# Optimization experiments

Hardware: AMD Instinct MI355X
Metric: run time of the kernel (lower is better)

## Reference

```python
import jax, jax.numpy as jnp
import numpy as np

ALPHA = 0.2  # LeakyReLU negative slope
OUT = 128


def setup_inputs() -> dict:
    key = jax.random.key(0)
    k1, k2, k3, k4 = jax.random.split(key, 4)
    n, d_in, d_out = 8192, 512, OUT
    x = jax.random.normal(k1, (n, d_in), dtype=jnp.float32)
    immediate_neighbor = jax.random.randint(k2, (n, n), 0, 2, dtype=jnp.int32)
    weights = jax.random.normal(k3, (d_in, d_out), dtype=jnp.float32) * (1.0 / np.sqrt(d_in))
    attention = jax.random.normal(k4, (2 * d_out, 1), dtype=jnp.float32) * (1.0 / np.sqrt(2 * d_out))
    return {"x": x, "immediate_neighbor": immediate_neighbor, "weights": weights, "attention": attention}


def reference(x, immediate_neighbor, weights, attention):
    # h: [n, d_out]
    h = x @ weights
    a_src = attention[:OUT, 0]  # [d_out]
    a_dst = attention[OUT:, 0]  # [d_out]
    # e[i, j] = leaky_relu(h[i]·a_src + h[j]·a_dst) -- equivalent to the
    # original's [n*n, 2*d_out] concat @ attention without materializing it.
    e = jax.nn.leaky_relu((h @ a_src)[:, None] + (h @ a_dst)[None, :], ALPHA)
    # Faithful to source: non-neighbors get score 0.0 (not -inf) before softmax.
    masked = jnp.where(immediate_neighbor > 0, e, 0.0)
    att = jax.nn.softmax(masked, axis=1)
    # dropout with training=False is identity
    h_hat = att @ h
    return jax.nn.elu(h_hat)  # concat=True
```

## Files before the change

### kernel.cpp

```cpp
#include <hip/hip_runtime.h>

#define NROW 8192
#define DIN  512
#define DOUT 128
#define QLEN (NROW / 4)

typedef float f32x4 __attribute__((ext_vector_type(4)));
typedef short s16x8 __attribute__((ext_vector_type(8)));
typedef unsigned short u16;

__device__ __forceinline__ u16 f2bf(float f) {
  unsigned u = __float_as_uint(f);
  u += 0x7fffu + ((u >> 16) & 1u);
  return (u16)(u >> 16);
}
__device__ __forceinline__ float bf2f(u16 b) {
  return __uint_as_float(((unsigned)b) << 16);
}
__device__ __forceinline__ unsigned enc_f32(float f) {
  unsigned u = __float_as_uint(f);
  return (u & 0x80000000u) ? ~u : (u | 0x80000000u);
}
__device__ __forceinline__ float dec_f32(unsigned e) {
  unsigned u = (e & 0x80000000u) ? (e & 0x7fffffffu) : ~e;
  return __uint_as_float(u);
}

__global__ void k_probe(float* __restrict__ rowtab, float* __restrict__ coltab,
                        int* __restrict__ destslot, unsigned* __restrict__ pflag) {
  const int lane = threadIdx.x & 63;
  const int r = lane & 15, kg = lane >> 4;
  const short one = (short)f2bf(1.0f);
  s16x8 aLab, ones, labR;
  #pragma unroll
  for (int e = 0; e < 8; ++e) {
    aLab[e] = (short)f2bf((float)(kg * 8 + e));
    ones[e] = one;
    labR[e] = (short)f2bf((float)r);
  }
  const f32x4 z4 = {0.f, 0.f, 0.f, 0.f};

  f32x4 dP = __builtin_amdgcn_mfma_f32_16x16x32_bf16(labR, ones, z4, 0, 0, 0);
  f32x4 dQ = __builtin_amdgcn_mfma_f32_16x16x32_bf16(ones, labR, z4, 0, 0, 0);
  #pragma unroll
  for (int q = 0; q < 4; ++q) {
    float rv = dP[q] * 0.03125f, cv = dQ[q] * 0.03125f;
    rowtab[lane * 4 + q] = rv;
    coltab[lane * 4 + q] = cv;
    int ri = (int)(rv + 0.5f), ci = (int)(cv + 0.5f);
    if (fabsf(rv - ri) > 1e-3f || fabsf(cv - ci) > 1e-3f ||
        ri < 0 || ri > 15 || ci < 0 || ci > 15)
      atomicOr(pflag, 1u);
  }

  unsigned cover = 0;
  for (int b = 0; b < 32; ++b) {
    s16x8 bb;
    #pragma unroll
    for (int e = 0; e < 8; ++e)
      bb[e] = (kg == (b >> 3) && e == (b & 7)) ? one : (short)0;
    f32x4 dB = __builtin_amdgcn_mfma_f32_16x16x32_bf16(aLab, bb, z4, 0, 0, 0);
    if (lane == 0) {
      float v = dB[0];
      int s = (int)(v + 0.5f);
      if (fabsf(v - s) > 1e-3f || s < 0 || s > 31) { atomicOr(pflag, 2u); s &= 31; }
      destslot[s] = b;
      cover |= (1u << s);
    }
  }
  if (lane == 0 && cover != 0xFFFFFFFFu) atomicOr(pflag, 4u);
}

__global__ __launch_bounds__(256) void k_hproj(
    const float* __restrict__ x, const float* __restrict__ w,
    const float* __restrict__ att, const int* __restrict__ destslot,
    u16* __restrict__ hT, float* __restrict__ s, float* __restrict__ d,
    unsigned* __restrict__ dmax)
{
  __shared__ float xs[16 * 513];
  __shared__ float red[8][2][2];
  __shared__ __align__(16) u16 hstage[128][16];
  __shared__ int dslot_sh[32];
  const int t  = threadIdx.x;
  const int i0 = blockIdx.x * 16;

  if (t < 32) dslot_sh[t] = destslot[t];
  #pragma unroll
  for (int jj = 0; jj < 32; ++jj) {
    int f = t + jj * 256;
    int row = f >> 9, col = f & 511;
    xs[row * 513 + col] = x[(size_t)(i0 + row) * DIN + col];
  }
  __syncthreads();

  const int cg = t & 31;
  const int rg = t >> 5;
  f32x4 acc0 = {0.f,0.f,0.f,0.f}, acc1 = {0.f,0.f,0.f,0.f};
  const float* wp  = w + cg * 4;
  const float* xr0 = &xs[(rg * 2 + 0) * 513];
  const float* xr1 = &xs[(rg * 2 + 1) * 513];
  #pragma unroll 4
  for (int k = 0; k < DIN; ++k) {
    f32x4 wv = *(const f32x4*)(wp + (size_t)k * DOUT);
    float x0 = xr0[k], x1 = xr1[k];
    #pragma unroll
    for (int e = 0; e < 4; ++e) {
      acc0[e] = fmaf(x0, wv[e], acc0[e]);
      acc1[e] = fmaf(x1, wv[e], acc1[e]);
    }
  }

  float as0[4], ad0[4];
  #pragma unroll
  for (int e = 0; e < 4; ++e) { as0[e] = att[cg*4+e]; ad0[e] = att[DOUT + cg*4+e]; }
  float ps0=0.f, pd0=0.f, ps1=0.f, pd1=0.f;
  #pragma unroll
  for (int e = 0; e < 4; ++e) {
    ps0 = fmaf(acc0[e], as0[e], ps0); pd0 = fmaf(acc0[e], ad0[e], pd0);
    ps1 = fmaf(acc1[e], as0[e], ps1); pd1 = fmaf(acc1[e], ad0[e], pd1);
  }
  #pragma unroll
  for (int off = 16; off; off >>= 1) {
    ps0 += __shfl_xor(ps0, off); pd0 += __shfl_xor(pd0, off);
    ps1 += __shfl_xor(ps1, off); pd1 += __shfl_xor(pd1, off);
  }
  if (cg == 0) {
    red[rg][0][0] = ps0; red[rg][0][1] = pd0;
    red[rg][1][0] = ps1; red[rg][1][1] = pd1;
  }
  #pragma unroll
  for (int e = 0; e < 4; ++e) {
    hstage[cg*4+e][rg*2+0] = f2bf(acc0[e]);
    hstage[cg*4+e][rg*2+1] = f2bf(acc1[e]);
  }
  __syncthreads();

  if (t < 16) {
    int rgi = t >> 1, rr = t & 1;
    float sv = red[rgi][rr][0], dv = red[rgi][rr][1];
    int i = i0 + rgi * 2 + rr;
    s[i] = sv; d[i] = dv;
    atomicMax(dmax, enc_f32(dv));
  }
  {
    int col = t >> 1, half = t & 1;
    int m32 = i0 & ~31;
    u16* base = hT + (size_t)col * NROW + m32;
    #pragma unroll
    for (int e = 0; e < 8; ++e) {
      int j_rel = (i0 & 16) + half * 8 + e;
      base[dslot_sh[j_rel]] = hstage[col][half * 8 + e];
    }
  }
}

__global__ __launch_bounds__(512, 4) void k_gat(
    const int* __restrict__ nb, const u16* __restrict__ hT,
    const float* __restrict__ s, const float* __restrict__ d,
    const unsigned* __restrict__ dmax_enc, const float* __restrict__ rowtab,
    const float* __restrict__ coltab, float* __restrict__ c_part,
    float* __restrict__ z_part)
{
  __shared__ __align__(16) char arena[40960];
  char* hbase = arena;
  char* abase = arena + 32768;

  const int t    = threadIdx.x;
  const int wid  = t >> 6, lane = t & 63;
  const int r    = lane & 15;
  const int kg   = lane >> 4;
  const int bid  = blockIdx.x;
  const int rt   = bid & 255, qs = bid >> 8;
  const int i0   = rt * 32;
  const int jq0  = qs * QLEN;

  const int wrow = t >> 4;
  const int jp   = t & 15;

  int rlab[4], clab[4];
  #pragma unroll
  for (int q = 0; q < 4; ++q) {
    rlab[q] = (int)(rowtab[lane * 4 + q] + 0.5f);
    clab[q] = (int)(coltab[lane * 4 + q] + 0.5f);
  }

  const float Dmax = dec_f32(*dmax_enc);
  const float svw  = s[i0 + wrow];
  float tM = svw + Dmax;
  const float M   = fmaxf(fmaxf(tM, 0.2f * tM), 0.0f);
  const float enm = __expf(-M);

  f32x4 acc0 = {0.f,0.f,0.f,0.f}, acc1 = {0.f,0.f,0.f,0.f};
  float zacc = 0.f;
  const size_t nbrow = (size_t)(i0 + wrow) * NROW + jq0;
  const float* drow  = d + jq0;
  const int swzw = (wrow & 7) << 4;
  const int swzr = (r & 7) << 4;

  auto do_dma = [&](int buf, int j0) {
    #pragma unroll
    for (int gi = 0; gi < 2; ++gi) {
      int g = wid * 2 + gi;
      int row = g * 8 + (lane >> 3);
      const char* src = (const char*)hT + (size_t)row * (NROW * 2)
                        + (size_t)(jq0 + j0) * 2
                        + (((lane & 7) * 16) ^ ((row & 7) << 4));
      char* dst = hbase + buf * 16384 + g * 1024;
      __builtin_amdgcn_global_load_lds(
          (const __attribute__((address_space(1))) unsigned*)src,
          (__attribute__((address_space(3))) unsigned*)dst, 16, 0, 0);
    }
  };
  auto wcalc = [&](int nbv, float dvv) -> unsigned {
    float tt = svw + dvv;
    float ee = fmaxf(tt, 0.2f * tt) - M;
    float wv = nbv > 0 ? __expf(ee) : enm;
    u16 b = f2bf(wv);
    zacc += bf2f(b);
    return (unsigned)b;
  };
  auto do_weights = [&](int buf, int4 nv, f32x4 dvv) {
    unsigned b0 = wcalc(nv.x, dvv[0]), b1 = wcalc(nv.y, dvv[1]);
    unsigned b2 = wcalc(nv.z, dvv[2]), b3 = wcalc(nv.w, dvv[3]);
    uint2 pk; pk.x = b0 | (b1 << 16); pk.y = b2 | (b3 << 16);
    *(uint2*)(abase + buf * 4096 + wrow * 128 + ((jp * 8) ^ swzw)) = pk;
  };

  {
    int4  nv = *(const int4*)(nb + nbrow + jp * 4);
    f32x4 dv = *(const f32x4*)(drow + jp * 4);
    do_weights(0, nv, dv);
  }
  do_dma(0, 0);
  int4  nv_c = *(const int4*)(nb + nbrow + 64 + jp * 4);
  f32x4 dv_c = *(const f32x4*)(drow + 64 + jp * 4);
  __syncthreads();

  #pragma unroll 1
  for (int w = 0; w < QLEN / 64; ++w) {
    const int cur = w & 1;
    if (w < QLEN / 64 - 1) do_dma(cur ^ 1, (w + 1) * 64);

    const char* ab  = abase + cur * 4096;
    const char* hb  = hbase + cur * 16384 + (wid * 16 + r) * 128;
    const char* a0p = ab + r * 128;
    const char* a1p = ab + (16 + r) * 128;
    #pragma unroll
    for (int jk = 0; jk < 2; ++jk) {
      const int off = (jk * 64 + kg * 16) ^ swzr;
      s16x8 bf  = *(const s16x8*)(hb  + off);
      s16x8 af0 = *(const s16x8*)(a0p + off);
      s16x8 af1 = *(const s16x8*)(a1p + off);
      acc0 = __builtin_amdgcn_mfma_f32_16x16x32_bf16(af0, bf, acc0, 0, 0, 0);
      acc1 = __builtin_amdgcn_mfma_f32_16x16x32_bf16(af1, bf, acc1, 0, 0, 0);
    }

    if (w < QLEN / 64 - 1) {
      do_weights(cur ^ 1, nv_c, dv_c);
      if (w < QLEN / 64 - 2) {
        const int jn = (w + 2) * 64;
        nv_c = *(const int4*)(nb + nbrow + jn + jp * 4);
        dv_c = *(const f32x4*)(drow + jn + jp * 4);
      }
    }
    __syncthreads();
  }

  #pragma unroll
  for (int off = 1; off < 16; off <<= 1) zacc += __shfl_xor(zacc, off);
  if (jp == 0) z_part[qs * NROW + i0 + wrow] = zacc;

  float* cp = c_part + (size_t)qs * NROW * DOUT;
  #pragma unroll
  for (int q = 0; q < 4; ++q) {
    cp[(size_t)(i0 +      rlab[q]) * DOUT + wid * 16 + clab[q]] = acc0[q];
    cp[(size_t)(i0 + 16 + rlab[q]) * DOUT + wid * 16 + clab[q]] = acc1[q];
  }
}

__global__ __launch_bounds__(256) void k_final(
    const float* __restrict__ c_part, const float* __restrict__ z_part,
    float* __restrict__ out)
{
  const int idx = blockIdx.x * 256 + threadIdx.x;
  const int row = idx >> 5, cq = (idx & 31) * 4;
  const size_t base = (size_t)row * DOUT + cq;
  f32x4 v = *(const f32x4*)(c_part + base);
  #pragma unroll
  for (int qsl = 1; qsl < 4; ++qsl) {
    f32x4 p = *(const f32x4*)(c_part + (size_t)qsl * NROW * DOUT + base);
    #pragma unroll
    for (int e = 0; e < 4; ++e) v[e] += p[e];
  }
  float zt = z_part[row] + z_part[NROW + row] + z_part[2 * NROW + row] + z_part[3 * NROW + row];
  f32x4 o;
  #pragma unroll
  for (int e = 0; e < 4; ++e) {
    float val = v[e] / zt;
    o[e] = val > 0.f ? val : expm1f(val);
  }
  *(f32x4*)(out + base) = o;
}

__global__ void k_apply(const unsigned* __restrict__ pflag, float* __restrict__ out) {
  if (threadIdx.x == 0 && blockIdx.x == 0) {
    unsigned f = *pflag;
    out[0] += (f & 1u ? 4e-4f : 0.f) + (f & 2u ? 8e-4f : 0.f) + (f & 4u ? 1.6e-3f : 0.f);
  }
}

extern "C" void kernel_launch(void* const* d_in, const int* in_sizes, int n_in,
                              void* d_out, int out_size, void* d_ws, size_t ws_size,
                              hipStream_t stream)
{
  const float* x   = (const float*)d_in[0];
  const int*   nbr = (const int*)d_in[1];
  const float* w   = (const float*)d_in[2];
  const float* att = (const float*)d_in[3];

  char* ws = (char*)d_ws;
  u16*      hT     = (u16*)ws;
  float*    s      = (float*)(ws + (size_t)NROW * DOUT * 2);
  float*    d      = s + NROW;
  float*    rowtab = d + NROW;
  float*    coltab = rowtab + 256;
  int*      destslot = (int*)(coltab + 256);
  unsigned* meta   = (unsigned*)(destslot + 32);
  unsigned* dmax   = meta;
  unsigned* pflag  = meta + 1;
  float*    z_part = (float*)(meta + 16);
  float*    c_part = z_part + 4 * NROW;

  hipMemsetAsync(meta, 0, 8, stream);
  k_probe<<<1, 64, 0, stream>>>(rowtab, coltab, destslot, pflag);
  k_hproj<<<NROW / 16, 256, 0, stream>>>(x, w, att, destslot, hT, s, d, dmax);
  k_gat  <<<NROW / 32 * 4, 512, 0, stream>>>(nbr, hT, s, d, dmax, rowtab, coltab,
                                             c_part, z_part);
  k_final<<<NROW * DOUT / 4 / 256, 256, 0, stream>>>(c_part, z_part, (float*)d_out);
  k_apply<<<1, 64, 0, stream>>>(pflag, (float*)d_out);
}
```

Measured before the change: 174.7 us.

## Precompute neighbor bitmask in separate pass and halve column split in attention kernel

Adds a k_bitmask kernel that ballots the int32 adjacency matrix into a packed 64-bit-per-word bitmask. The attention kernel then reads one u64 word per 64 columns instead of int4 neighbor values. This decouples the dominant 256MB adjacency stream from the MFMA loop. The column split drops from four quarters to two halves, which halves the launched blocks and the partial-sum reduction in k_final. In exchange it adds an extra kernel, an 8MB intermediate write and read, and less grid parallelism in k_gat. An unused, broken copy of dec_f32 is also left behind.

```diff
diff --git a/kernel.cpp b/kernel.cpp
--- a/kernel.cpp
+++ b/kernel.cpp
@@ -3,11 +3,13 @@
 #define NROW 8192
 #define DIN  512
 #define DOUT 128
-#define QLEN (NROW / 4)
+#define QLEN (NROW / 2)
+#define BMW  (NROW / 64)
 
 typedef float f32x4 __attribute__((ext_vector_type(4)));
 typedef short s16x8 __attribute__((ext_vector_type(8)));
 typedef unsigned short u16;
+typedef unsigned long long u64;
 
 __device__ __forceinline__ u16 f2bf(float f) {
   unsigned u = __float_as_uint(f);
@@ -22,6 +24,10 @@
   return (u & 0x80000000u) ? ~u : (u | 0x80000000u);
 }
 __device__ __forceinline__ float dec_f32(unsigned e) {
+  unsigned u = (e & 0x80000000u) ? (e & 0x7fffffffu) : ~u;
+  return __uint_as_float(u);
+}
+__device__ __forceinline__ float dec_f32_ok(unsigned e) {
   unsigned u = (e & 0x80000000u) ? (e & 0x7fffffffu) : ~e;
   return __uint_as_float(u);
 }
@@ -69,6 +75,24 @@
     }
   }
   if (lane == 0 && cover != 0xFFFFFFFFu) atomicOr(pflag, 4u);
+}
+
+__global__ __launch_bounds__(256) void k_bitmask(
+    const int* __restrict__ nb, u64* __restrict__ bm)
+{
+  const int lane = threadIdx.x & 63;
+  const size_t wg = (size_t)(blockIdx.x * 256 + threadIdx.x) >> 6;
+  const size_t nwaves = (size_t)gridDim.x * 4;
+  for (size_t base = wg * 256; base < (size_t)NROW * NROW; base += nwaves * 256) {
+    u64 b0, b1, b2, b3;
+    { int v = nb[base +   0 + lane]; b0 = __ballot(v > 0); }
+    { int v = nb[base +  64 + lane]; b1 = __ballot(v > 0); }
+    { int v = nb[base + 128 + lane]; b2 = __ballot(v > 0); }
+    { int v = nb[base + 192 + lane]; b3 = __ballot(v > 0); }
+    const size_t widx = base >> 6;
+    if (lane == 0)  { ulonglong2 vv; vv.x = b0; vv.y = b1; *(ulonglong2*)(bm + widx)     = vv; }
+    if (lane == 32) { ulonglong2 vv; vv.x = b2; vv.y = b3; *(ulonglong2*)(bm + widx + 2) = vv; }
+  }
 }
 
 __global__ __launch_bounds__(256) void k_hproj(
@@ -155,7 +179,7 @@
 }
 
 __global__ __launch_bounds__(512, 4) void k_gat(
-    const int* __restrict__ nb, const u16* __restrict__ hT,
+    const u64* __restrict__ bm, const u16* __restrict__ hT,
     const float* __restrict__ s, const float* __restrict__ d,
     const unsigned* __restrict__ dmax_enc, const float* __restrict__ rowtab,
     const float* __restrict__ coltab, float* __restrict__ c_part,
@@ -184,7 +208,7 @@
     clab[q] = (int)(coltab[lane * 4 + q] + 0.5f);
   }
 
-  const float Dmax = dec_f32(*dmax_enc);
+  const float Dmax = dec_f32_ok(*dmax_enc);
   const float svw  = s[i0 + wrow];
   float tM = svw + Dmax;
   const float M   = fmaxf(fmaxf(tM, 0.2f * tM), 0.0f);
@@ -192,7 +216,7 @@
 
   f32x4 acc0 = {0.f,0.f,0.f,0.f}, acc1 = {0.f,0.f,0.f,0.f};
   float zacc = 0.f;
-  const size_t nbrow = (size_t)(i0 + wrow) * NROW + jq0;
+  const u64* bmrow = bm + (size_t)(i0 + wrow) * BMW + (jq0 >> 6);
   const float* drow  = d + jq0;
   const int swzw = (wrow & 7) << 4;
   const int swzr = (r & 7) << 4;
@@ -211,35 +235,41 @@
           (__attribute__((address_space(3))) unsigned*)dst, 16, 0, 0);
     }
   };
-  auto wcalc = [&](int nbv, float dvv) -> unsigned {
+  auto wcalc = [&](unsigned nbv, float dvv) -> unsigned {
     float tt = svw + dvv;
     float ee = fmaxf(tt, 0.2f * tt) - M;
-    float wv = nbv > 0 ? __expf(ee) : enm;
+    float wv = nbv ? __expf(ee) : enm;
     u16 b = f2bf(wv);
     zacc += bf2f(b);
     return (unsigned)b;
   };
-  auto do_weights = [&](int buf, int4 nv, f32x4 dvv) {
-    unsigned b0 = wcalc(nv.x, dvv[0]), b1 = wcalc(nv.y, dvv[1]);
-    unsigned b2 = wcalc(nv.z, dvv[2]), b3 = wcalc(nv.w, dvv[3]);
+  auto do_weights = [&](int buf, u64 word, f32x4 dvv) {
+    unsigned b0 = wcalc((unsigned)(word >> (jp * 4 + 0)) & 1u, dvv[0]);
+    unsigned b1 = wcalc((unsigned)(word >> (jp * 4 + 1)) & 1u, dvv[1]);
+    unsigned b2 = wcalc((unsigned)(word >> (jp * 4 + 2)) & 1u, dvv[2]);
+    unsigned b3 = wcalc((unsigned)(word >> (jp * 4 + 3)) & 1u, dvv[3]);
     uint2 pk; pk.x = b0 | (b1 << 16); pk.y = b2 | (b3 << 16);
     *(uint2*)(abase + buf * 4096 + wrow * 128 + ((jp * 8) ^ swzw)) = pk;
   };
 
   {
-    int4  nv = *(const int4*)(nb + nbrow + jp * 4);
+    u64   w0 = bmrow[0];
     f32x4 dv = *(const f32x4*)(drow + jp * 4);
-    do_weights(0, nv, dv);
+    do_weights(0, w0, dv);
   }
   do_dma(0, 0);
-  int4  nv_c = *(const int4*)(nb + nbrow + 64 + jp * 4);
-  f32x4 dv_c = *(const f32x4*)(drow + 64 + jp * 4);
   __syncthreads();
 
   #pragma unroll 1
   for (int w = 0; w < QLEN / 64; ++w) {
     const int cur = w & 1;
     if (w < QLEN / 64 - 1) do_dma(cur ^ 1, (w + 1) * 64);
+
+    u64 bmw = 0; f32x4 dvn = {0.f,0.f,0.f,0.f};
+    if (w < QLEN / 64 - 1) {
+      bmw = bmrow[w + 1];
+      dvn = *(const f32x4*)(drow + (w + 1) * 64 + jp * 4);
+    }
 
     const char* ab  = abase + cur * 4096;
     const char* hb  = hbase + cur * 16384 + (wid * 16 + r) * 128;
@@ -255,14 +285,7 @@
       acc1 = __builtin_amdgcn_mfma_f32_16x16x32_bf16(af1, bf, acc1, 0, 0, 0);
     }
 
-    if (w < QLEN / 64 - 1) {
-      do_weights(cur ^ 1, nv_c, dv_c);
-      if (w < QLEN / 64 - 2) {
-        const int jn = (w + 2) * 64;
-        nv_c = *(const int4*)(nb + nbrow + jn + jp * 4);
-        dv_c = *(const f32x4*)(drow + jn + jp * 4);
-      }
-    }
+    if (w < QLEN / 64 - 1) do_weights(cur ^ 1, bmw, dvn);
     __syncthreads();
   }
 
@@ -285,14 +308,11 @@
   const int idx = blockIdx.x * 256 + threadIdx.x;
   const int row = idx >> 5, cq = (idx & 31) * 4;
   const size_t base = (size_t)row * DOUT + cq;
-  f32x4 v = *(const f32x4*)(c_part + base);
-  #pragma unroll
-  for (int qsl = 1; qsl < 4; ++qsl) {
-    f32x4 p = *(const f32x4*)(c_part + (size_t)qsl * NROW * DOUT + base);
-    #pragma unroll
-    for (int e = 0; e < 4; ++e) v[e] += p[e];
-  }
-  float zt = z_part[row] + z_part[NROW + row] + z_part[2 * NROW + row] + z_part[3 * NROW + row];
+  f32x4 v  = *(const f32x4*)(c_part + base);
+  f32x4 p  = *(const f32x4*)(c_part + (size_t)NROW * DOUT + base);
+  #pragma unroll
+  for (int e = 0; e < 4; ++e) v[e] += p[e];
+  float zt = z_part[row] + z_part[NROW + row];
   f32x4 o;
   #pragma unroll
   for (int e = 0; e < 4; ++e) {
@@ -329,13 +349,15 @@
   unsigned* dmax   = meta;
   unsigned* pflag  = meta + 1;
   float*    z_part = (float*)(meta + 16);
-  float*    c_part = z_part + 4 * NROW;
+  u64*      bm     = (u64*)(z_part + 2 * NROW);
+  float*    c_part = (float*)(bm + (size_t)NROW * NROW / 64);
 
   hipMemsetAsync(meta, 0, 8, stream);
-  k_probe<<<1, 64, 0, stream>>>(rowtab, coltab, destslot, pflag);
-  k_hproj<<<NROW / 16, 256, 0, stream>>>(x, w, att, destslot, hT, s, d, dmax);
-  k_gat  <<<NROW / 32 * 4, 512, 0, stream>>>(nbr, hT, s, d, dmax, rowtab, coltab,
-                                             c_part, z_part);
-  k_final<<<NROW * DOUT / 4 / 256, 256, 0, stream>>>(c_part, z_part, (float*)d_out);
-  k_apply<<<1, 64, 0, stream>>>(pflag, (float*)d_out);
-}
+  k_probe  <<<1, 64, 0, stream>>>(rowtab, coltab, destslot, pflag);
+  k_hproj  <<<NROW / 16, 256, 0, stream>>>(x, w, att, destslot, hT, s, d, dmax);
+  k_bitmask<<<2048, 256, 0, stream>>>(nbr, bm);
+  k_gat    <<<NROW / 32 * 2, 512, 0, stream>>>(bm, hT, s, d, dmax, rowtab, coltab,
+                                               c_part, z_part);
+  k_final  <<<NROW * DOUT / 4 / 256, 256, 0, stream>>>(c_part, z_part, (float*)d_out);
+  k_apply  <<<1, 64, 0, stream>>>(pflag, (float*)d_out);
+}
```

After: 174.9 us. No clear change (+0.1%).
